# Optimization experiments

Hardware: AMD Instinct MI355X
Metric: run time of the kernel (lower is better)

Reference implementation:

```python
import jax, jax.numpy as jnp
import numpy as np
from jax import lax

B, T = 128, 128
MODEL = 128          # model_size = hidden_size = cell_size (w)
R = 4                # read heads
M = 64               # nr_cells
W = MODEL            # cell size
VOCAB = 512
CLIP = 20.0          # dnc default controller clip
DELTA = 1e-6         # dnc epsilon
IFACE = R * W + 3 * W + 5 * R + 3  # 919 interface outputs


def setup_inputs():
    key = jax.random.key(0)
    ks = jax.random.split(key, 12)
    g = lambda k, s, sc: jax.random.normal(k, s, dtype=jnp.float32) * sc
    H = MODEL
    return {
        'tokens': jax.random.randint(ks[0], (B, T), 0, VOCAB),
        'emb': g(ks[1], (VOCAB, MODEL), 0.02),
        # controller: 2-layer LSTM, layer0 input = model + r*w
        'w_ih0': g(ks[2], (4 * H, MODEL + R * W), 0.05),
        'w_hh0': g(ks[3], (4 * H, H), 0.05),
        'b_ih0': jnp.zeros((4 * H,), jnp.float32),
        'b_hh0': jnp.zeros((4 * H,), jnp.float32),
        'w_ih1': g(ks[4], (4 * H, H), 0.05),
        'w_hh1': g(ks[5], (4 * H, H), 0.05),
        'b_ih1': jnp.zeros((4 * H,), jnp.float32),
        'b_hh1': jnp.zeros((4 * H,), jnp.float32),
        # memory interface linear: hidden -> 919
        'w_iface': g(ks[6], (IFACE, H), 0.05),
        'b_iface': jnp.zeros((IFACE,), jnp.float32),
        # dnc output linear: (hidden + r*w) -> model
        'w_out': g(ks[7], (MODEL, H + R * W), 0.05),
        'b_out': jnp.zeros((MODEL,), jnp.float32),
        # DNCAE fc head: model -> vocab
        'w_fc': g(ks[8], (VOCAB, MODEL), 0.05),
        'b_fc': jnp.zeros((VOCAB,), jnp.float32),
        # dnc initializes controller h (and c = h.clone()) with xavier-uniform noise
        'h0': g(ks[9], (2, B, H), 0.1),
    }


def _lstm_step(x, h, c, w_ih, w_hh, b_ih, b_hh):
    gates = x @ w_ih.T + b_ih + h @ w_hh.T + b_hh
    i, f, g, o = jnp.split(gates, 4, axis=-1)  # pytorch gate order i,f,g,o
    c2 = jax.nn.sigmoid(f) * c + jax.nn.sigmoid(i) * jnp.tanh(g)
    h2 = jax.nn.sigmoid(o) * jnp.tanh(c2)
    return h2, c2


def _cosine(mem, keys):
    # mem (B,M,W), keys (B,K,W) -> similarity (B,K,M); dnc adds DELTA to norms
    mn = mem / (jnp.linalg.norm(mem, axis=2, keepdims=True) + DELTA)
    kn = keys / (jnp.linalg.norm(keys, axis=2, keepdims=True) + DELTA)
    return jnp.einsum('bmw,bkw->bkm', mn, kn)


def _dnc_forward(tokens, emb, w_ih0, w_hh0, b_ih0, b_hh0, w_ih1, w_hh1, b_ih1,
                 b_hh1, w_iface, b_iface, w_out, b_out, w_fc, b_fc, h0):
    x = emb[tokens]  # (B,T,MODEL)
    # ixaxaar dnc concatenates the *initial* last_read (zeros) to every timestep input
    xs = jnp.concatenate([x, jnp.zeros((B, T, R * W), x.dtype)], axis=-1)
    eye_mask = 1.0 - jnp.eye(M, dtype=x.dtype)

    def step(carry, x_t):
        hl0, hl1, cl0, cl1, mem, link, prec, rw, ww, usage = carry
        nh0, nc0 = _lstm_step(x_t, hl0, cl0, w_ih0, w_hh0, b_ih0, b_hh0)
        nh1, nc1 = _lstm_step(nh0, hl1, cl1, w_ih1, w_hh1, b_ih1, b_hh1)
        out = jnp.clip(nh1, -CLIP, CLIP)
        xi = out @ w_iface.T + b_iface  # (B, 919)
        o = R * W
        read_keys = jnp.tanh(xi[:, :R * W]).reshape(B, R, W)
        read_str = jax.nn.softplus(xi[:, o:o + R]); o += R
        write_key = jnp.tanh(xi[:, o:o + W]).reshape(B, 1, W); o += W
        write_str = jax.nn.softplus(xi[:, o:o + 1]); o += 1
        erase = jax.nn.sigmoid(xi[:, o:o + W]); o += W
        write_vec = jnp.tanh(xi[:, o:o + W]); o += W
        free_gates = jax.nn.sigmoid(xi[:, o:o + R]); o += R
        alloc_gate = jax.nn.sigmoid(xi[:, o:o + 1]); o += 1
        write_gate = jax.nn.sigmoid(xi[:, o:o + 1]); o += 1
        read_modes = jax.nn.softmax(xi[:, o:o + 3 * R].reshape(B, R, 3), axis=2)

        # ---- write phase ----
        # usage (single write head: 1-prod(1-ww) == ww)
        usage = usage + (1.0 - usage) * ww
        psi = jnp.prod(1.0 - free_gates[:, :, None] * rw, axis=1)  # (B,M)
        usage = usage * psi
        # content weighting on pre-write memory
        wcw = jax.nn.softmax(_cosine(mem, write_key) * write_str[:, :, None], axis=2)[:, 0, :]
        # allocation weighting via sorted-usage cumprod
        u = DELTA + (1.0 - DELTA) * usage
        phi = jnp.argsort(u, axis=1)
        sorted_u = jnp.take_along_axis(u, phi, axis=1)
        prod_su = jnp.cumprod(jnp.concatenate([jnp.ones((B, 1), u.dtype), sorted_u], axis=1), axis=1)[:, :-1]
        sorted_alloc = (1.0 - sorted_u) * prod_su
        alloc = jnp.take_along_axis(sorted_alloc, jnp.argsort(phi, axis=1), axis=1)
        # final write weighting (B,M)
        ww = write_gate * (alloc_gate * alloc + (1.0 - alloc_gate) * wcw)
        # erase + write memory
        mem = mem * (1.0 - ww[:, :, None] * erase[:, None, :]) + ww[:, :, None] * write_vec[:, None, :]
        # temporal link matrix
        ww_i = ww[:, :, None]
        ww_j = ww[:, None, :]
        link = (1.0 - ww_i - ww_j) * link + ww_i * prec[:, None, :]
        link = link * eye_mask
        prec = (1.0 - jnp.sum(ww, axis=1, keepdims=True)) * prec + ww

        # ---- read phase (on post-write memory) ----
        cw = jax.nn.softmax(_cosine(mem, read_keys) * read_str[:, :, None], axis=2)  # (B,R,M)
        fwd = jnp.einsum('bij,brj->bri', link, rw)
        bwd = jnp.einsum('bri,bij->brj', rw, link)
        rw = read_modes[:, :, 0:1] * bwd + read_modes[:, :, 1:2] * fwd + read_modes[:, :, 2:3] * cw
        read_vecs = jnp.einsum('brm,bmw->brw', rw, mem).reshape(B, R * W)

        y = jnp.concatenate([out, read_vecs], axis=-1) @ w_out.T + b_out  # (B,MODEL)
        return (nh0, nh1, nc0, nc1, mem, link, prec, rw, ww, usage), y

    z = jnp.zeros
    carry0 = (h0[0], h0[1], h0[0], h0[1],
              z((B, M, W), jnp.float32), z((B, M, M), jnp.float32), z((B, M), jnp.float32),
              z((B, R, M), jnp.float32), z((B, M), jnp.float32), z((B, M), jnp.float32))
    _, ys = lax.scan(step, carry0, jnp.swapaxes(xs, 0, 1))  # ys (T,B,MODEL)
    dnc_out = jnp.swapaxes(ys, 0, 1)  # (B,T,MODEL)
    logits = dnc_out @ w_fc.T + b_fc  # (B,T,VOCAB)
    return jnp.transpose(logits, (0, 2, 1))  # (B,VOCAB,T) like .permute(0,2,1)


def reference(tokens, emb, w_ih0, w_hh0, b_ih0, b_hh0, w_ih1, w_hh1, b_ih1,
              b_hh1, w_iface, b_iface, w_out, b_out, w_fc, b_fc, h0):
    return _dnc_forward(tokens, emb, w_ih0, w_hh0, b_ih0, b_hh0, w_ih1, w_hh1,
                        b_ih1, b_hh1, w_iface, b_iface, w_out, b_out, w_fc, b_fc, h0)
```

## Files before the change

### kernel.cpp

```cpp
#include <hip/hip_runtime.h>
#include <math.h>

#define B 128
#define T 128
#define H 128
#define RH 4
#define M 64
#define W 128
#define VOCAB 512
#define IFACE 919
#define G4 512
#define DELTA 1e-6f
#define CLIPV 20.0f

#define MEMLD 132
#define LNKLD 67
#define CH 8
#define XILD 928

__device__ __forceinline__ float sigmoidf_(float x){ return 1.0f/(1.0f+expf(-x)); }
__device__ __forceinline__ float softplusf_(float x){
  return fmaxf(x, 0.0f) + log1pf(expf(-fabsf(x)));
}
__device__ __forceinline__ float waveAllSum(float v){
  for (int off=1; off<64; off<<=1) v += __shfl_xor(v, off, 64);
  return v;
}
__device__ __forceinline__ float waveAllMax(float v){
  for (int off=1; off<64; off<<=1) v = fmaxf(v, __shfl_xor(v, off, 64));
  return v;
}

__global__ void k_transpose(const float* __restrict__ in, float* __restrict__ out,
                            int rows, int cols, int use_cols){
  int idx = blockIdx.x*blockDim.x + threadIdx.x;
  int total = rows*use_cols;
  if (idx < total){
    int r = idx / use_cols, c = idx - r*use_cols;
    out[c*rows + r] = in[r*cols + c];
  }
}

__global__ void k_xw0(const float* __restrict__ emb, const float* __restrict__ wih0T,
                      const float* __restrict__ b_ih0, const float* __restrict__ b_hh0,
                      float* __restrict__ xw0){
  __shared__ float e[H];
  int v = blockIdx.x, g = threadIdx.x;
  if (g < H) e[g] = emb[v*H + g];
  __syncthreads();
  float acc = b_ih0[g] + b_hh0[g];
  #pragma unroll 8
  for (int k=0;k<H;k++) acc += e[k]*wih0T[k*G4 + g];
  xw0[v*G4 + g] = acc;
}

__launch_bounds__(512, 1)
__global__ void k_tail(const float* __restrict__ stash, const float* __restrict__ w_out,
                       const float* __restrict__ b_out, const float* __restrict__ w_fc,
                       const float* __restrict__ b_fc, float* __restrict__ out){
  __shared__ __align__(16) float S[32*644];
  __shared__ float Y[32*129];
  const int tid = threadIdx.x;
  const long bt0 = (long)blockIdx.x*32;

  for (int idx = tid; idx < 32*640; idx += 512){
    int bt = idx / 640, k = idx - bt*640;
    S[bt*644 + k] = stash[(bt0+bt)*640 + k];
  }
  __syncthreads();
  {
    int og = tid >> 5, bt = tid & 31;
    const float4* s4 = (const float4*)(S + bt*644);
    #pragma unroll
    for (int oo = 0; oo < 8; ++oo){
      int o = og*8 + oo;
      const float4* w4 = (const float4*)(w_out + (size_t)o*640);
      float acc = b_out[o];
      #pragma unroll 8
      for (int k4 = 0; k4 < 160; ++k4){
        float4 w = w4[k4], s = s4[k4];
        acc += w.x*s.x + w.y*s.y + w.z*s.z + w.w*s.w;
      }
      Y[bt*129 + o] = acc;
    }
  }
  __syncthreads();
  {
    int t = tid & 31, vg = tid >> 5;
    int b  = (int)(bt0 >> 7);
    int tb = (int)(bt0 & 127);
    const float* yr = Y + t*129;
    #pragma unroll 2
    for (int vv = 0; vv < 32; ++vv){
      int v = vg*32 + vv;
      const float4* w4 = (const float4*)(w_fc + (size_t)v*H);
      float acc = b_fc[v];
      #pragma unroll 8
      for (int k4 = 0; k4 < 32; ++k4){
        float4 w = w4[k4];
        int k = k4*4;
        acc += w.x*yr[k] + w.y*yr[k+1] + w.z*yr[k+2] + w.w*yr[k+3];
      }
      out[((size_t)b*VOCAB + v)*T + tb + t] = acc;
    }
  }
}

__launch_bounds__(512, 1)
__global__ void k_dnc(const int* __restrict__ tokens,
                      const float* __restrict__ xw0,
                      const float* __restrict__ whh0T,
                      const float* __restrict__ w1catT,
                      const float* __restrict__ b_ih1,
                      const float* __restrict__ b_hh1,
                      const float* __restrict__ wifaceT,
                      const float* __restrict__ b_iface,
                      const float* __restrict__ h0,
                      float* __restrict__ outg,
                      float* __restrict__ stash,
                      unsigned* __restrict__ flags)
{
  const int role = blockIdx.x >> 7;
  const int b = blockIdx.x & 127;
  const int tid = threadIdx.x;
  const int lane = tid & 63;
  const int wave = tid >> 6;

  __shared__ __align__(16) float hcat[2*H];
  __shared__ __align__(16) float c0s[H], c1s[H];
  __shared__ __align__(16) float mem[M*MEMLD];
  __shared__ float link[M*LNKLD];
  __shared__ float prec[M], ww[M], usage[M];
  __shared__ float rw[RH*M];
  __shared__ __align__(16) float gates[G4];
  __shared__ __align__(16) float rk[RH*W];
  __shared__ float wk[W], er[W], wv[W];
  __shared__ float memnorm[M];
  __shared__ float wcw[M], alloc_s[M];
  __shared__ float cwm[RH*M], fwd[RH*M], bwd[RH*M];
  __shared__ int   tok[T];
  __shared__ float rstr[RH], rmode[RH*3];
  __shared__ float s_wstr, s_ag, s_wg, s_wwsum, s_wkinv, s_rkinv[RH];
  __shared__ __align__(16) float xi_chunk[CH*XILD];
  __shared__ __align__(16) float out_s[CH*H];

  if (role == 0){
    const float b1sum = b_ih1[tid] + b_hh1[tid];
    if (tid < H){
      float hv0 = h0[0*B*H + b*H + tid];
      float hv1 = h0[1*B*H + b*H + tid];
      hcat[tid]=hv0; hcat[H+tid]=hv1; c0s[tid]=hv0; c1s[tid]=hv1;
    }
    if (tid < T) tok[tid] = tokens[b*T + tid];
    __syncthreads();

    for (int t = 0; t < T; ++t){
      {
        float acc = xw0[(size_t)tok[t]*G4 + tid];
        const float* wp = whh0T + tid;
        #pragma unroll 8
        for (int k=0;k<H;k++) acc += hcat[k]*wp[k*G4];
        gates[tid] = acc;
      }
      __syncthreads();
      if (tid < H){
        float ig = sigmoidf_(gates[tid]);
        float ff = sigmoidf_(gates[H+tid]);
        float gg = tanhf(gates[2*H+tid]);
        float og = sigmoidf_(gates[3*H+tid]);
        float c2 = ff*c0s[tid] + ig*gg;
        c0s[tid] = c2;
        hcat[tid] = og*tanhf(c2);
      }
      __syncthreads();
      {
        float acc = b1sum;
        const float* wp1 = w1catT + tid;
        const float* wp2 = w1catT + 128*G4 + tid;
        #pragma unroll 4
        for (int k=0;k<H;k++) acc += hcat[k]*wp1[k*G4] + hcat[H+k]*wp2[k*G4];
        gates[tid] = acc;
      }
      __syncthreads();
      if (tid < H){
        float ig = sigmoidf_(gates[tid]);
        float ff = sigmoidf_(gates[H+tid]);
        float gg = tanhf(gates[2*H+tid]);
        float og = sigmoidf_(gates[3*H+tid]);
        float c2 = ff*c1s[tid] + ig*gg;
        c1s[tid] = c2;
        float h2 = og*tanhf(c2);
        hcat[H+tid] = h2;
        float ov = fminf(fmaxf(h2, -CLIPV), CLIPV);
        const long bt = (long)b*T + t;
        outg[bt*H + tid] = ov;
        stash[bt*640 + tid] = ov;
      }
      __syncthreads();
      if ((t & (CH-1)) == CH-1){
        if (tid == 0)
          __hip_atomic_store(&flags[b], (unsigned)((t>>3)+1),
                             __ATOMIC_RELEASE, __HIP_MEMORY_SCOPE_AGENT);
      }
    }
  } else {
    const bool  two = (tid < IFACE-512);
    const float bi0 = b_iface[tid];
    const float bi1 = two ? b_iface[tid+512] : 0.f;

    for (int i = tid; i < M*MEMLD; i += 512) mem[i]=0.f;
    for (int i = tid; i < M*LNKLD; i += 512) link[i]=0.f;
    if (tid < M){ prec[tid]=0.f; ww[tid]=0.f; usage[tid]=0.f; }
    if (tid < RH*M) rw[tid]=0.f;
    __syncthreads();

    for (int c = 0; c < T/CH; ++c){
      if (tid == 0){
        while (__hip_atomic_load(&flags[b], __ATOMIC_ACQUIRE,
                                 __HIP_MEMORY_SCOPE_AGENT) < (unsigned)(c+1))
          __builtin_amdgcn_s_sleep(4);
      }
      __syncthreads();

      for (int idx = tid; idx < CH*H; idx += 512)
        out_s[idx] = outg[((size_t)b*T + c*CH)*H + idx];
      __syncthreads();

      {
        float a0[CH], a1[CH];
        #pragma unroll
        for (int r=0;r<CH;r++){ a0[r] = bi0; a1[r] = bi1; }
        const float* wp1 = wifaceT + tid;
        const float* wp2 = wifaceT + tid + 512;
        #pragma unroll 4
        for (int k=0;k<H;k++){
          float w1 = wp1[k*IFACE];
          float w2 = two ? wp2[k*IFACE] : 0.f;
          #pragma unroll
          for (int r=0;r<CH;r++){
            float o = out_s[r*H + k];
            a0[r] += o*w1;
            a1[r] += o*w2;
          }
        }
        #pragma unroll
        for (int r=0;r<CH;r++){
          xi_chunk[r*XILD + tid] = a0[r];
          if (two) xi_chunk[r*XILD + tid + 512] = a1[r];
        }
      }
      __syncthreads();

      for (int s = 0; s < CH; ++s){
        const int t = c*CH + s;
        const long bt = (long)b*T + t;
        const float* xc = xi_chunk + s*XILD;

        rk[tid] = tanhf(xc[tid]);
        if (tid < W){
          wk[tid] = tanhf(xc[516+tid]);
          er[tid] = sigmoidf_(xc[645+tid]);
          wv[tid] = tanhf(xc[773+tid]);
        }
        if (tid < RH){
          rstr[tid] = softplusf_(xc[512+tid]);
          float a0 = xc[907+3*tid], a1 = xc[908+3*tid], a2 = xc[909+3*tid];
          float mx = fmaxf(a0, fmaxf(a1,a2));
          float e0=expf(a0-mx), e1=expf(a1-mx), e2=expf(a2-mx);
          float s3 = e0+e1+e2;
          rmode[3*tid]=e0/s3; rmode[3*tid+1]=e1/s3; rmode[3*tid+2]=e2/s3;
        }
        if (tid == 0){
          s_wstr = softplusf_(xc[644]);
          s_ag = sigmoidf_(xc[905]);
          s_wg = sigmoidf_(xc[906]);
        }
        if (tid < M){
          float f0 = sigmoidf_(xc[901]);
          float f1 = sigmoidf_(xc[902]);
          float f2 = sigmoidf_(xc[903]);
          float f3 = sigmoidf_(xc[904]);
          float um = usage[tid] + (1.0f-usage[tid])*ww[tid];
          float psi = (1.0f - f0*rw[tid])      * (1.0f - f1*rw[M+tid])
                    * (1.0f - f2*rw[2*M+tid])  * (1.0f - f3*rw[3*M+tid]);
          usage[tid] = um*psi;
        }
        {
          int row = tid >> 3, sub = tid & 7;
          float ss = 0.f;
          #pragma unroll
          for (int i=0;i<16;i++){ float v = mem[row*MEMLD + sub + 8*i]; ss += v*v; }
          ss += __shfl_down(ss,4,8); ss += __shfl_down(ss,2,8); ss += __shfl_down(ss,1,8);
          if (sub==0) memnorm[row] = 1.0f/(sqrtf(ss)+DELTA);
        }
        if (wave == 0){
          float v0 = tanhf(xc[516+lane]), v1 = tanhf(xc[516+lane+64]);
          float ss = waveAllSum(v0*v0+v1*v1);
          if (lane==0) s_wkinv = 1.0f/(sqrtf(ss)+DELTA);
        } else if (wave <= RH){
          int r = wave-1;
          float v0 = tanhf(xc[r*W+lane]), v1 = tanhf(xc[r*W+lane+64]);
          float ss = waveAllSum(v0*v0+v1*v1);
          if (lane==0) s_rkinv[r] = 1.0f/(sqrtf(ss)+DELTA);
        }
        __syncthreads();

        {
          int m = tid >> 3, sub = tid & 7;
          float d = 0.f;
          #pragma unroll
          for (int i=0;i<16;i++){ int e = sub + 8*i; d += mem[m*MEMLD + e]*wk[e]; }
          d += __shfl_down(d,4,8); d += __shfl_down(d,2,8); d += __shfl_down(d,1,8);
          if (sub==0) wcw[m] = d * memnorm[m] * s_wkinv * s_wstr;
        }
        __syncthreads();

        if (wave == 0){
          float x = wcw[lane];
          float mx = waveAllMax(x);
          float e = expf(x-mx);
          float s2 = waveAllSum(e);
          wcw[lane] = e/s2;
        } else if (wave == 1){
          float u = DELTA + (1.0f-DELTA)*usage[lane];
          int idx = lane;
          for (int k=2;k<=64;k<<=1){
            for (int j=k>>1;j>0;j>>=1){
              float ou = __shfl_xor(u, j, 64);
              int   oi = __shfl_xor(idx, j, 64);
              bool up = ((lane & k) == 0);
              bool iLower = ((lane & j) == 0);
              bool otherLess = (ou < u) || (ou == u && oi < idx);
              bool takeOther = (up == iLower) ? otherLess : !otherLess;
              if (takeOther){ u = ou; idx = oi; }
            }
          }
          float p = u;
          for (int d=1; d<64; d<<=1){
            float pv = __shfl_up(p, d, 64);
            if (lane >= d) p *= pv;
          }
          float ep = __shfl_up(p, 1, 64);
          if (lane == 0) ep = 1.0f;
          alloc_s[idx] = (1.0f - u) * ep;
        }
        __syncthreads();

        if (tid < M){
          float wwm = s_wg*(s_ag*alloc_s[tid] + (1.0f-s_ag)*wcw[tid]);
          ww[tid] = wwm;
          float s2 = waveAllSum(wwm);
          if (lane==0) s_wwsum = s2;
        }
        __syncthreads();

        #pragma unroll
        for (int e=0;e<16;e++){
          int f = tid + 512*e;
          int m = f >> 7, w = f & 127;
          mem[m*MEMLD+w] = mem[m*MEMLD+w]*(1.0f - ww[m]*er[w]) + ww[m]*wv[w];
        }
        #pragma unroll
        for (int e=0;e<8;e++){
          int f = tid + 512*e;
          int i = f >> 6, j = f & 63;
          float lv = (1.0f - ww[i] - ww[j])*link[i*LNKLD+j] + ww[i]*prec[j];
          link[i*LNKLD+j] = (i==j) ? 0.0f : lv;
        }
        __syncthreads();

        if (tid < M) prec[tid] = (1.0f - s_wwsum)*prec[tid] + ww[tid];
        {
          int row = tid >> 3, sub = tid & 7;
          float ss = 0.f;
          #pragma unroll
          for (int i=0;i<16;i++){ float v = mem[row*MEMLD + sub + 8*i]; ss += v*v; }
          ss += __shfl_down(ss,4,8); ss += __shfl_down(ss,2,8); ss += __shfl_down(ss,1,8);
          if (sub==0) memnorm[row] = 1.0f/(sqrtf(ss)+DELTA);
        }
        __syncthreads();

        {
          int r = tid >> 7, m = (tid >> 1) & 63, sub = tid & 1;
          float d = 0.f;
          #pragma unroll 8
          for (int i=0;i<64;i++){ int e = sub + 2*i; d += mem[m*MEMLD + e]*rk[r*W + e]; }
          d += __shfl_down(d,1,2);
          if (sub==0) cwm[r*M+m] = d * memnorm[m] * s_rkinv[r] * rstr[r];
        }
        if (tid < 256){
          int r = tid >> 6, i = tid & 63;
          float a = 0.f;
          #pragma unroll 8
          for (int j=0;j<M;j++) a += link[i*LNKLD+j]*rw[r*M+j];
          fwd[r*M+i] = a;
        } else {
          int q = tid - 256;
          int r = q >> 6, j = q & 63;
          float a = 0.f;
          #pragma unroll 8
          for (int i=0;i<M;i++) a += rw[r*M+i]*link[i*LNKLD+j];
          bwd[r*M+j] = a;
        }
        __syncthreads();

        if (wave < RH){
          int r = wave;
          float x = cwm[r*M + lane];
          float mx = waveAllMax(x);
          float e = expf(x-mx);
          float s2 = waveAllSum(e);
          float cc = e/s2;
          rw[r*M+lane] = rmode[3*r]*bwd[r*M+lane] + rmode[3*r+1]*fwd[r*M+lane]
                       + rmode[3*r+2]*cc;
        }
        __syncthreads();

        {
          int r = tid >> 7, w = tid & 127;
          float a = 0.f;
          #pragma unroll 8
          for (int m=0;m<M;m++) a += rw[r*M+m]*mem[m*MEMLD+w];
          stash[bt*640 + 128 + tid] = a;
        }
        __syncthreads();
      }
    }
  }
}

extern "C" void kernel_launch(void* const* d_in, const int* in_sizes, int n_in,
                              void* d_out, int out_size, void* d_ws, size_t ws_size,
                              hipStream_t stream)
{
  const int*   tokens  = (const int*)d_in[0];
  const float* emb     = (const float*)d_in[1];
  const float* w_ih0   = (const float*)d_in[2];
  const float* w_hh0   = (const float*)d_in[3];
  const float* b_ih0   = (const float*)d_in[4];
  const float* b_hh0   = (const float*)d_in[5];
  const float* w_ih1   = (const float*)d_in[6];
  const float* w_hh1   = (const float*)d_in[7];
  const float* b_ih1   = (const float*)d_in[8];
  const float* b_hh1   = (const float*)d_in[9];
  const float* w_iface = (const float*)d_in[10];
  const float* b_iface = (const float*)d_in[11];
  const float* w_out   = (const float*)d_in[12];
  const float* b_out   = (const float*)d_in[13];
  const float* w_fc    = (const float*)d_in[14];
  const float* b_fc    = (const float*)d_in[15];
  const float* h0      = (const float*)d_in[16];
  float* out = (float*)d_out;
  float* ws  = (float*)d_ws;

  float* xw0     = ws;
  float* whh0T   = xw0     + 262144;
  float* w1catT  = whh0T   + 65536;
  float* wifaceT = w1catT  + 131072;
  float* wih0T   = wifaceT + 117632;
  float* stash   = wih0T   + 65536;
  float* outg    = stash   + 10485760;
  unsigned* flags = (unsigned*)(outg + 2097152);

  auto tp = [&](const float* in, float* o, int rows, int cols, int use){
    int total = rows*use;
    k_transpose<<<(total+255)/256, 256, 0, stream>>>(in, o, rows, cols, use);
  };
  tp(w_ih0,   wih0T,          512, 640, 128);
  tp(w_hh0,   whh0T,          512, 128, 128);
  tp(w_ih1,   w1catT,         512, 128, 128);
  tp(w_hh1,   w1catT+128*G4,  512, 128, 128);
  tp(w_iface, wifaceT,        919, 128, 128);
  k_xw0<<<VOCAB, 512, 0, stream>>>(emb, wih0T, b_ih0, b_hh0, xw0);
  hipMemsetAsync(flags, 0, 128*sizeof(unsigned), stream);
  k_dnc<<<2*B, 512, 0, stream>>>(tokens, xw0, whh0T, w1catT, b_ih1, b_hh1,
                                 wifaceT, b_iface, h0, outg, stash, flags);
  k_tail<<<(B*T)/32, 512, 0, stream>>>(stash, w_out, b_out, w_fc, b_fc, out);
}
```

Before: 2.501 ms.

## Move interface projection to LSTM producer block with double-buffered handoff

The interface linear projection per 8-step chunk moves from the memory (consumer) block to the LSTM (producer) block. It writes into a double-buffered global slot guarded by producer and consumer flags, so the consumer only copies precomputed values into shared memory. The intent is to shorten the consumer's serial critical path, which bounds total time. Separately, the write-weight computation is fused into the memory and link update to drop a barrier, the wwsum and prec updates move onto idle waves, and the mem row stride is padded to 133 to reduce bank conflicts. The cost is more work on the producer and a backpressure wait that could stall it.

```diff
diff --git a/kernel.cpp b/kernel.cpp
--- a/kernel.cpp
+++ b/kernel.cpp
@@ -13,7 +13,7 @@
 #define DELTA 1e-6f
 #define CLIPV 20.0f
 
-#define MEMLD 132
+#define MEMLD 133
 #define LNKLD 67
 #define CH 8
 #define XILD 928
@@ -116,9 +116,10 @@
                       const float* __restrict__ wifaceT,
                       const float* __restrict__ b_iface,
                       const float* __restrict__ h0,
-                      float* __restrict__ outg,
+                      float* __restrict__ xibuf,
                       float* __restrict__ stash,
-                      unsigned* __restrict__ flags)
+                      unsigned* __restrict__ pflag,
+                      unsigned* __restrict__ cflag)
 {
   const int role = blockIdx.x >> 7;
   const int b = blockIdx.x & 127;
@@ -146,6 +147,10 @@
 
   if (role == 0){
     const float b1sum = b_ih1[tid] + b_hh1[tid];
+    const bool  two = (tid < IFACE-512);
+    const float bi0 = b_iface[tid];
+    const float bi1 = two ? b_iface[tid+512] : 0.f;
+
     if (tid < H){
       float hv0 = h0[0*B*H + b*H + tid];
       float hv1 = h0[1*B*H + b*H + tid];
@@ -154,79 +159,63 @@
     if (tid < T) tok[tid] = tokens[b*T + tid];
     __syncthreads();
 
-    for (int t = 0; t < T; ++t){
+    for (int c = 0; c < T/CH; ++c){
+      for (int s = 0; s < CH; ++s){
+        const int t = c*CH + s;
+        {
+          float acc = xw0[(size_t)tok[t]*G4 + tid];
+          const float* wp = whh0T + tid;
+          #pragma unroll 8
+          for (int k=0;k<H;k++) acc += hcat[k]*wp[k*G4];
+          gates[tid] = acc;
+        }
+        __syncthreads();
+        if (tid < H){
+          float ig = sigmoidf_(gates[tid]);
+          float ff = sigmoidf_(gates[H+tid]);
+          float gg = tanhf(gates[2*H+tid]);
+          float og = sigmoidf_(gates[3*H+tid]);
+          float c2 = ff*c0s[tid] + ig*gg;
+          c0s[tid] = c2;
+          hcat[tid] = og*tanhf(c2);
+        }
+        __syncthreads();
+        {
+          float acc = b1sum;
+          const float* wp1 = w1catT + tid;
+          const float* wp2 = w1catT + 128*G4 + tid;
+          #pragma unroll 4
+          for (int k=0;k<H;k++) acc += hcat[k]*wp1[k*G4] + hcat[H+k]*wp2[k*G4];
+          gates[tid] = acc;
+        }
+        __syncthreads();
+        if (tid < H){
+          float ig = sigmoidf_(gates[tid]);
+          float ff = sigmoidf_(gates[H+tid]);
+          float gg = tanhf(gates[2*H+tid]);
+          float og = sigmoidf_(gates[3*H+tid]);
+          float c2 = ff*c1s[tid] + ig*gg;
+          c1s[tid] = c2;
+          float h2 = og*tanhf(c2);
+          hcat[H+tid] = h2;
+          float ov = fminf(fmaxf(h2, -CLIPV), CLIPV);
+          out_s[s*H + tid] = ov;
+          stash[((long)b*T + t)*640 + tid] = ov;
+        }
+        __syncthreads();
+      }
+
+      if (c >= 2){
+        if (tid == 0){
+          while (__hip_atomic_load(&cflag[b], __ATOMIC_ACQUIRE,
+                                   __HIP_MEMORY_SCOPE_AGENT) < (unsigned)(c-1))
+            __builtin_amdgcn_s_sleep(2);
+        }
+        __syncthreads();
+      }
+
       {
-        float acc = xw0[(size_t)tok[t]*G4 + tid];
-        const float* wp = whh0T + tid;
-        #pragma unroll 8
-        for (int k=0;k<H;k++) acc += hcat[k]*wp[k*G4];
-        gates[tid] = acc;
-      }
-      __syncthreads();
-      if (tid < H){
-        float ig = sigmoidf_(gates[tid]);
-        float ff = sigmoidf_(gates[H+tid]);
-        float gg = tanhf(gates[2*H+tid]);
-        float og = sigmoidf_(gates[3*H+tid]);
-        float c2 = ff*c0s[tid] + ig*gg;
-        c0s[tid] = c2;
-        hcat[tid] = og*tanhf(c2);
-      }
-      __syncthreads();
-      {
-        float acc = b1sum;
-        const float* wp1 = w1catT + tid;
-        const float* wp2 = w1catT + 128*G4 + tid;
-        #pragma unroll 4
-        for (int k=0;k<H;k++) acc += hcat[k]*wp1[k*G4] + hcat[H+k]*wp2[k*G4];
-        gates[tid] = acc;
-      }
-      __syncthreads();
-      if (tid < H){
-        float ig = sigmoidf_(gates[tid]);
-        float ff = sigmoidf_(gates[H+tid]);
-        float gg = tanhf(gates[2*H+tid]);
-        float og = sigmoidf_(gates[3*H+tid]);
-        float c2 = ff*c1s[tid] + ig*gg;
-        c1s[tid] = c2;
-        float h2 = og*tanhf(c2);
-        hcat[H+tid] = h2;
-        float ov = fminf(fmaxf(h2, -CLIPV), CLIPV);
-        const long bt = (long)b*T + t;
-        outg[bt*H + tid] = ov;
-        stash[bt*640 + tid] = ov;
-      }
-      __syncthreads();
-      if ((t & (CH-1)) == CH-1){
-        if (tid == 0)
-          __hip_atomic_store(&flags[b], (unsigned)((t>>3)+1),
-                             __ATOMIC_RELEASE, __HIP_MEMORY_SCOPE_AGENT);
-      }
-    }
-  } else {
-    const bool  two = (tid < IFACE-512);
-    const float bi0 = b_iface[tid];
-    const float bi1 = two ? b_iface[tid+512] : 0.f;
-
-    for (int i = tid; i < M*MEMLD; i += 512) mem[i]=0.f;
-    for (int i = tid; i < M*LNKLD; i += 512) link[i]=0.f;
-    if (tid < M){ prec[tid]=0.f; ww[tid]=0.f; usage[tid]=0.f; }
-    if (tid < RH*M) rw[tid]=0.f;
-    __syncthreads();
-
-    for (int c = 0; c < T/CH; ++c){
-      if (tid == 0){
-        while (__hip_atomic_load(&flags[b], __ATOMIC_ACQUIRE,
-                                 __HIP_MEMORY_SCOPE_AGENT) < (unsigned)(c+1))
-          __builtin_amdgcn_s_sleep(4);
-      }
-      __syncthreads();
-
-      for (int idx = tid; idx < CH*H; idx += 512)
-        out_s[idx] = outg[((size_t)b*T + c*CH)*H + idx];
-      __syncthreads();
-
-      {
+        float* xslot = xibuf + ((size_t)b*2 + (c&1))*(CH*XILD);
         float a0[CH], a1[CH];
         #pragma unroll
         for (int r=0;r<CH;r++){ a0[r] = bi0; a1[r] = bi1; }
@@ -245,11 +234,39 @@
         }
         #pragma unroll
         for (int r=0;r<CH;r++){
-          xi_chunk[r*XILD + tid] = a0[r];
-          if (two) xi_chunk[r*XILD + tid + 512] = a1[r];
+          xslot[r*XILD + tid] = a0[r];
+          if (two) xslot[r*XILD + tid + 512] = a1[r];
         }
       }
       __syncthreads();
+      if (tid == 0)
+        __hip_atomic_store(&pflag[b], (unsigned)(c+1),
+                           __ATOMIC_RELEASE, __HIP_MEMORY_SCOPE_AGENT);
+    }
+  } else {
+    for (int i = tid; i < M*MEMLD; i += 512) mem[i]=0.f;
+    for (int i = tid; i < M*LNKLD; i += 512) link[i]=0.f;
+    if (tid < M){ prec[tid]=0.f; ww[tid]=0.f; usage[tid]=0.f; }
+    if (tid < RH*M) rw[tid]=0.f;
+    __syncthreads();
+
+    for (int c = 0; c < T/CH; ++c){
+      if (tid == 0){
+        while (__hip_atomic_load(&pflag[b], __ATOMIC_ACQUIRE,
+                                 __HIP_MEMORY_SCOPE_AGENT) < (unsigned)(c+1))
+          __builtin_amdgcn_s_sleep(4);
+      }
+      __syncthreads();
+
+      {
+        const float4* src = (const float4*)(xibuf + ((size_t)b*2 + (c&1))*(CH*XILD));
+        float4* dst = (float4*)xi_chunk;
+        for (int i = tid; i < CH*XILD/4; i += 512) dst[i] = src[i];
+      }
+      __syncthreads();
+      if (tid == 0)
+        __hip_atomic_store(&cflag[b], (unsigned)(c+1),
+                           __ATOMIC_RELEASE, __HIP_MEMORY_SCOPE_AGENT);
 
       for (int s = 0; s < CH; ++s){
         const int t = c*CH + s;
@@ -346,30 +363,28 @@
         }
         __syncthreads();
 
-        if (tid < M){
-          float wwm = s_wg*(s_ag*alloc_s[tid] + (1.0f-s_ag)*wcw[tid]);
-          ww[tid] = wwm;
-          float s2 = waveAllSum(wwm);
-          if (lane==0) s_wwsum = s2;
-        }
-        __syncthreads();
-
-        #pragma unroll
-        for (int e=0;e<16;e++){
-          int f = tid + 512*e;
-          int m = f >> 7, w = f & 127;
-          mem[m*MEMLD+w] = mem[m*MEMLD+w]*(1.0f - ww[m]*er[w]) + ww[m]*wv[w];
-        }
-        #pragma unroll
-        for (int e=0;e<8;e++){
-          int f = tid + 512*e;
-          int i = f >> 6, j = f & 63;
-          float lv = (1.0f - ww[i] - ww[j])*link[i*LNKLD+j] + ww[i]*prec[j];
-          link[i*LNKLD+j] = (i==j) ? 0.0f : lv;
-        }
-        __syncthreads();
-
-        if (tid < M) prec[tid] = (1.0f - s_wwsum)*prec[tid] + ww[tid];
+        {
+          const float cg = s_wg, ag = s_ag;
+          #pragma unroll
+          for (int e=0;e<16;e++){
+            int f = tid + 512*e;
+            int m = f >> 7, w = f & 127;
+            float wwm = cg*(ag*alloc_s[m] + (1.0f-ag)*wcw[m]);
+            mem[m*MEMLD+w] = mem[m*MEMLD+w]*(1.0f - wwm*er[w]) + wwm*wv[w];
+          }
+          #pragma unroll
+          for (int e=0;e<8;e++){
+            int f = tid + 512*e;
+            int i = f >> 6, j = f & 63;
+            float wwi = cg*(ag*alloc_s[i] + (1.0f-ag)*wcw[i]);
+            float wwj = cg*(ag*alloc_s[j] + (1.0f-ag)*wcw[j]);
+            float lv = (1.0f - wwi - wwj)*link[i*LNKLD+j] + wwi*prec[j];
+            link[i*LNKLD+j] = (i==j) ? 0.0f : lv;
+          }
+          if (tid < M) ww[tid] = cg*(ag*alloc_s[tid] + (1.0f-ag)*wcw[tid]);
+        }
+        __syncthreads();
+
         {
           int row = tid >> 3, sub = tid & 7;
           float ss = 0.f;
@@ -402,6 +417,10 @@
           for (int i=0;i<M;i++) a += rw[r*M+i]*link[i*LNKLD+j];
           bwd[r*M+j] = a;
         }
+        if (wave == 7){
+          float s2 = waveAllSum(ww[lane]);
+          if (lane==0) s_wwsum = s2;
+        }
         __syncthreads();
 
         if (wave < RH){
@@ -413,6 +432,8 @@
           float cc = e/s2;
           rw[r*M+lane] = rmode[3*r]*bwd[r*M+lane] + rmode[3*r+1]*fwd[r*M+lane]
                        + rmode[3*r+2]*cc;
+        } else if (wave == 4){
+          prec[lane] = (1.0f - s_wwsum)*prec[lane] + ww[lane];
         }
         __syncthreads();
 
@@ -459,8 +480,9 @@
   float* wifaceT = w1catT  + 131072;
   float* wih0T   = wifaceT + 117632;
   float* stash   = wih0T   + 65536;
-  float* outg    = stash   + 10485760;
-  unsigned* flags = (unsigned*)(outg + 2097152);
+  float* xibuf   = stash   + 10485760;
+  unsigned* pflag = (unsigned*)(xibuf + 1900544);
+  unsigned* cflag = pflag + 128;
 
   auto tp = [&](const float* in, float* o, int rows, int cols, int use){
     int total = rows*use;
@@ -472,8 +494,9 @@
   tp(w_hh1,   w1catT+128*G4,  512, 128, 128);
   tp(w_iface, wifaceT,        919, 128, 128);
   k_xw0<<<VOCAB, 512, 0, stream>>>(emb, wih0T, b_ih0, b_hh0, xw0);
-  hipMemsetAsync(flags, 0, 128*sizeof(unsigned), stream);
+  hipMemsetAsync(pflag, 0, 256*sizeof(unsigned), stream);
   k_dnc<<<2*B, 512, 0, stream>>>(tokens, xw0, whh0T, w1catT, b_ih1, b_hh1,
-                                 wifaceT, b_iface, h0, outg, stash, flags);
+                                 wifaceT, b_iface, h0, xibuf, stash,
+                                 pflag, cflag);
   k_tail<<<(B*T)/32, 512, 0, stream>>>(stash, w_out, b_out, w_fc, b_fc, out);
 }
```

Measured after the change: 2.372 ms, median of 2. 5.2% less time.
